# Kernel optimization log

Hardware: AMD Instinct MI355X
Metric: run time of the kernel (lower is better)

## Reference

```python
import jax, jax.numpy as jnp
import numpy as np

B, N, E = 128, 300, 300        # batch, nodes (max_length), edges per sample
DIN, DH, DOUT = 768, 256, 256  # input feat, gcn hidden, gcn output
R = 26                         # NUM_DEP_TYPES
NHEADS, HDIM = 8, DH // 8


def setup_inputs() -> dict:
    key = jax.random.key(0)
    ks = jax.random.split(key, 12)
    s = lambda d: 1.0 / np.sqrt(d)
    return {
        "node_features": jax.random.normal(ks[0], (B, N, DIN), jnp.float32),
        "src": jax.random.randint(ks[1], (B, E), 0, N, jnp.int32),
        "dst": jax.random.randint(ks[2], (B, E), 0, N, jnp.int32),
        "etype": jax.random.randint(ks[3], (B, E), 0, R, jnp.int32),
        "W_rel": jax.random.normal(ks[4], (R, DIN, DH), jnp.float32) * s(DIN),
        "W_loop": jax.random.normal(ks[5], (DIN, DH), jnp.float32) * s(DIN),
        "b_rel": jnp.zeros((DH,), jnp.float32),
        "in_proj_w": jax.random.normal(ks[6], (3 * DH, DH), jnp.float32) * s(DH),
        "in_proj_b": jnp.zeros((3 * DH,), jnp.float32),
        "out_proj_w": jax.random.normal(ks[7], (DH, DH), jnp.float32) * s(DH),
        "out_proj_b": jnp.zeros((DH,), jnp.float32),
        "mlp_w": jax.random.normal(ks[8], (DOUT, DH), jnp.float32) * s(DH),
        "mlp_b": jnp.zeros((DOUT,), jnp.float32),
    }


def reference(node_features, src, dst, etype, W_rel, W_loop, b_rel,
              in_proj_w, in_proj_b, out_proj_w, out_proj_b, mlp_w, mlp_b):
    # ---- RelGraphConv (regularizer=None, self_loop=True, sum aggregation) ----
    # gather source-node features per edge: [B, E, DIN]
    h_src = jnp.take_along_axis(node_features, src[..., None].astype(jnp.int32), axis=1)
    # per-relation masked matmul: msg[b,e] = h_src[b,e] @ W_rel[etype[b,e]]
    msg = jnp.zeros((B, E, DH), node_features.dtype)
    for r in range(R):  # fixed small relation set
        mask = (etype == r)[..., None]
        msg = msg + jnp.einsum('bei,io->beo', jnp.where(mask, h_src, 0.0), W_rel[r])
    # scatter-add messages to destination nodes
    b_idx = jnp.arange(B)[:, None]
    agg = jnp.zeros((B, N, DH), node_features.dtype).at[b_idx, dst].add(msg)
    h = agg + jnp.einsum('bni,io->bno', node_features, W_loop) + b_rel  # [B, N, DH]

    # ---- MultiheadAttention (self-attn over nodes, eval mode) ----
    qkv = jnp.einsum('bnd,ed->bne', h, in_proj_w) + in_proj_b
    q, k, v = jnp.split(qkv, 3, axis=-1)
    q = q.reshape(B, N, NHEADS, HDIM)
    k = k.reshape(B, N, NHEADS, HDIM)
    v = v.reshape(B, N, NHEADS, HDIM)
    scores = jnp.einsum('bqhd,bkhd->bhqk', q, k) / np.sqrt(HDIM)
    attn = jax.nn.softmax(scores, axis=-1)
    ctx = jnp.einsum('bhqk,bkhd->bqhd', attn, v).reshape(B, N, DH)
    attn_out = jnp.einsum('bnd,ed->bne', ctx, out_proj_w) + out_proj_b

    # ---- mean-pool over nodes + MLP ----
    pooled = jnp.mean(attn_out, axis=1)  # [B, DH]
    return pooled @ mlp_w.T + mlp_b      # [B, DOUT]
```

## Files before the change

kernel.cpp:

```cpp
#include <hip/hip_runtime.h>
#include <cstdint>
#include <cstddef>

#define BB 128
#define NN 300
#define EE 300
#define DIN 768
#define DH 256
#define NREL 26
#define NHEADS 8
#define HDIM 32
#define MTOT (BB*NN)
#define NEDGE (BB*EE)
#define NHB 150

typedef __attribute__((ext_vector_type(8))) short bf16x8;
typedef __attribute__((ext_vector_type(4))) float f32x4;
typedef unsigned short u16;
union BU { uint4 u; bf16x8 v; };

__device__ __forceinline__ unsigned int packbf2(float a, float b) {
    unsigned int ua = __float_as_uint(a);
    unsigned int ub = __float_as_uint(b);
    ua = (ua + 0x7FFFu + ((ua >> 16) & 1u)) >> 16;
    ub = (ub + 0x7FFFu + ((ub >> 16) & 1u)) & 0xFFFF0000u;
    return ua | ub;
}
__device__ __forceinline__ u16 packbf1(float a) {
    unsigned int ua = __float_as_uint(a);
    return (u16)((ua + 0x7FFFu + ((ua >> 16) & 1u)) >> 16);
}

__global__ __launch_bounds__(256) void b_hist(const int* __restrict__ etype,
                                              int* __restrict__ blockhist) {
    __shared__ int hist[NREL];
    const int tid = threadIdx.x;
    if (tid < NREL) hist[tid] = 0;
    __syncthreads();
    atomicAdd(&hist[etype[blockIdx.x * 256 + tid]], 1);
    __syncthreads();
    if (tid < NREL) blockhist[blockIdx.x * NREL + tid] = hist[tid];
}

__global__ __launch_bounds__(64) void b_scan(const int* __restrict__ blockhist,
                                             int* __restrict__ blockbase,
                                             int* __restrict__ cnt, int* __restrict__ off) {
    __shared__ int tot[NREL];
    const int r = threadIdx.x;
    if (r < NREL) {
        int run = 0;
        for (int b = 0; b < NHB; ++b) {
            blockbase[b * NREL + r] = run;
            run += blockhist[b * NREL + r];
        }
        tot[r] = run;
        cnt[r] = run;
    }
    __syncthreads();
    __shared__ int offs[NREL + 1];
    if (r == 0) {
        int acc = 0;
        for (int q = 0; q < NREL; ++q) { offs[q] = acc; off[q] = acc; acc += tot[q]; }
        offs[NREL] = acc; off[NREL] = acc;
    }
    __syncthreads();
    if (r < NREL) {
        int o = offs[r];
        for (int b = 0; b < NHB; ++b) blockbase[b * NREL + r] += o;
    }
}

__global__ __launch_bounds__(256) void b_scatter(const int* __restrict__ etype,
                                                 const int* __restrict__ blockbase,
                                                 int* __restrict__ list) {
    __shared__ int wavehist[4][NREL];
    __shared__ int waveoff[4][NREL];
    const int tid = threadIdx.x;
    const int w = tid >> 6, l = tid & 63;
    const int i = blockIdx.x * 256 + tid;
    const int r = etype[i];
    unsigned long long mymask = 0ull;
    #pragma unroll
    for (int q = 0; q < NREL; ++q) {
        unsigned long long m = __ballot(r == q);
        if (l == 0) wavehist[w][q] = __popcll(m);
        if (r == q) mymask = m;
    }
    const int myrank = __popcll(mymask & ((1ull << l) - 1ull));
    __syncthreads();
    if (tid < NREL) {
        int acc = 0;
        #pragma unroll
        for (int ww = 0; ww < 4; ++ww) { waveoff[ww][tid] = acc; acc += wavehist[ww][tid]; }
    }
    __syncthreads();
    list[blockbase[blockIdx.x * NREL + r] + waveoff[w][r] + myrank] = i;
}

__global__ __launch_bounds__(256) void c_cast8(const float4* __restrict__ in,
                                               uint4* __restrict__ out, int n8) {
    int i = blockIdx.x * 256 + threadIdx.x;
    if (i < n8) {
        float4 f0 = in[2*i], f1 = in[2*i+1];
        uint4 o;
        o.x = packbf2(f0.x, f0.y); o.y = packbf2(f0.z, f0.w);
        o.z = packbf2(f1.x, f1.y); o.w = packbf2(f1.z, f1.w);
        out[i] = o;
    }
}

__global__ __launch_bounds__(256) void c_cast_w(
    const float* __restrict__ wrel, const float* __restrict__ wl, const float* __restrict__ wq,
    uint4* __restrict__ wrb, uint4* __restrict__ wlb, uint4* __restrict__ wqb) {
    int t = blockIdx.x * 256 + threadIdx.x;
    int l = t & 63, fid = t >> 6;
    if (fid < NREL*24*16) {
        int r = fid / 384, rem = fid - r * 384;
        int kf = rem >> 4, nt = rem & 15;
        int k0 = 32*kf + 8*(l >> 4), n = 16*nt + (l & 15);
        const float* p = wrel + ((size_t)r*768 + k0) * 256 + n;
        uint4 o;
        o.x = packbf2(p[0], p[256]); o.y = packbf2(p[512], p[768]);
        o.z = packbf2(p[1024], p[1280]); o.w = packbf2(p[1536], p[1792]);
        wrb[t] = o;
    } else if (fid < NREL*24*16 + 384) {
        int f2 = fid - NREL*24*16;
        int kf = f2 >> 4, nt = f2 & 15;
        int k0 = 32*kf + 8*(l >> 4), n = 16*nt + (l & 15);
        const float* p = wl + (size_t)k0 * 256 + n;
        uint4 o;
        o.x = packbf2(p[0], p[256]); o.y = packbf2(p[512], p[768]);
        o.z = packbf2(p[1024], p[1280]); o.w = packbf2(p[1536], p[1792]);
        wlb[f2*64 + l] = o;
    } else {
        int f2 = fid - NREL*24*16 - 384;
        int kf = f2 / 48, nt = f2 % 48;
        int e = 16*nt + (l & 15), d0 = 32*kf + 8*(l >> 4);
        const float4* p = (const float4*)(wq + (size_t)e * 256 + d0);
        float4 f0 = p[0], f1 = p[1];
        uint4 o;
        o.x = packbf2(f0.x, f0.y); o.y = packbf2(f0.z, f0.w);
        o.z = packbf2(f1.x, f1.y); o.w = packbf2(f1.z, f1.w);
        wqb[f2*64 + l] = o;
    }
}

__global__ __launch_bounds__(256) void k1m(
    const uint4* __restrict__ xb, const uint4* __restrict__ wlb,
    const float* __restrict__ brel, float* __restrict__ h) {
    __shared__ uint4 As[512];
    const int tid = threadIdx.x;
    const int m0 = blockIdx.x * 64;
    const int nb = blockIdx.y;
    const int w = tid >> 6, l = tid & 63;
    const int g = l >> 4, q = l & 15;
    int cA[2];
    #pragma unroll
    for (int p = 0; p < 2; ++p) {
        int s = tid + p * 256;
        int fi = s >> 6, l2 = s & 63;
        int kf = fi >> 2, mt = fi & 3;
        int row = m0 + 16*mt + (l2 & 15);
        cA[p] = row * 96 + 4*kf + (l2 >> 4);
    }
    f32x4 acc[4][2];
    #pragma unroll
    for (int a = 0; a < 4; ++a)
        #pragma unroll
        for (int n = 0; n < 2; ++n) acc[a][n] = (f32x4){0.f,0.f,0.f,0.f};

    for (int step = 0; step < 12; ++step) {
        uint4 a0 = xb[cA[0] + step*8];
        uint4 a1 = xb[cA[1] + step*8];
        BU Bf[2][2];
        #pragma unroll
        for (int kf = 0; kf < 2; ++kf)
            #pragma unroll
            for (int nt = 0; nt < 2; ++nt)
                Bf[kf][nt].u = wlb[((step*2 + kf)*16 + nb*8 + w*2 + nt)*64 + l];
        __syncthreads();
        As[tid] = a0; As[tid + 256] = a1;
        __syncthreads();
        #pragma unroll
        for (int kf = 0; kf < 2; ++kf) {
            BU Af[4];
            #pragma unroll
            for (int mt = 0; mt < 4; ++mt) Af[mt].u = As[(kf*4 + mt)*64 + l];
            #pragma unroll
            for (int mt = 0; mt < 4; ++mt)
                #pragma unroll
                for (int nt = 0; nt < 2; ++nt)
                    acc[mt][nt] = __builtin_amdgcn_mfma_f32_16x16x32_bf16(Af[mt].v, Bf[kf][nt].v, acc[mt][nt], 0, 0, 0);
        }
    }
    #pragma unroll
    for (int nt = 0; nt < 2; ++nt) {
        int col = nb*128 + w*32 + nt*16 + q;
        float bias = brel[col];
        #pragma unroll
        for (int mt = 0; mt < 4; ++mt)
            #pragma unroll
            for (int i = 0; i < 4; ++i)
                h[(size_t)(m0 + 16*mt + 4*g + i)*256 + col] = acc[mt][nt][i] + bias;
    }
}

__global__ __launch_bounds__(256) void k2m(
    const uint4* __restrict__ xb, const uint4* __restrict__ wrb,
    const int* __restrict__ src, const int* __restrict__ dst,
    const int* __restrict__ cnt, const int* __restrict__ off,
    const int* __restrict__ list, float* __restrict__ h) {
    __shared__ uint4 As[512];
    __shared__ int arow_s[64];
    __shared__ int drow_s[64];
    const int r = blockIdx.y;
    const int c_total = cnt[r];
    const int t0 = blockIdx.x * 64;
    if (t0 >= c_total) return;
    const int nb = blockIdx.z;
    const int tid = threadIdx.x;
    if (tid < 64) {
        int e = t0 + tid;
        int ar = 0, dr = -1;
        if (e < c_total) {
            int eid = list[off[r] + e];
            int b = eid / EE;
            ar = b * NN + src[eid];
            dr = b * NN + dst[eid];
        }
        arow_s[tid] = ar; drow_s[tid] = dr;
    }
    __syncthreads();
    const int w = tid >> 6, l = tid & 63;
    const int g = l >> 4, q = l & 15;
    int cA[2];
    #pragma unroll
    for (int p = 0; p < 2; ++p) {
        int s = tid + p * 256;
        int fi = s >> 6, l2 = s & 63;
        int kf = fi >> 2, mt = fi & 3;
        int row = arow_s[16*mt + (l2 & 15)];
        cA[p] = row * 96 + 4*kf + (l2 >> 4);
    }
    const uint4* wb = wrb + (size_t)r * 24*16*64;
    f32x4 acc[4][2];
    #pragma unroll
    for (int a = 0; a < 4; ++a)
        #pragma unroll
        for (int n = 0; n < 2; ++n) acc[a][n] = (f32x4){0.f,0.f,0.f,0.f};

    for (int step = 0; step < 12; ++step) {
        uint4 a0 = xb[cA[0] + step*8];
        uint4 a1 = xb[cA[1] + step*8];
        BU Bf[2][2];
        #pragma unroll
        for (int kf = 0; kf < 2; ++kf)
            #pragma unroll
            for (int nt = 0; nt < 2; ++nt)
                Bf[kf][nt].u = wb[((step*2 + kf)*16 + nb*8 + w*2 + nt)*64 + l];
        __syncthreads();
        As[tid] = a0; As[tid + 256] = a1;
        __syncthreads();
        #pragma unroll
        for (int kf = 0; kf < 2; ++kf) {
            BU Af[4];
            #pragma unroll
            for (int mt = 0; mt < 4; ++mt) Af[mt].u = As[(kf*4 + mt)*64 + l];
            #pragma unroll
            for (int mt = 0; mt < 4; ++mt)
                #pragma unroll
                for (int nt = 0; nt < 2; ++nt)
                    acc[mt][nt] = __builtin_amdgcn_mfma_f32_16x16x32_bf16(Af[mt].v, Bf[kf][nt].v, acc[mt][nt], 0, 0, 0);
        }
    }
    #pragma unroll
    for (int mt = 0; mt < 4; ++mt)
        #pragma unroll
        for (int i = 0; i < 4; ++i) {
            int dr = drow_s[16*mt + 4*g + i];
            if (dr >= 0) {
                #pragma unroll
                for (int nt = 0; nt < 2; ++nt)
                    atomicAdd(&h[(size_t)dr*256 + nb*128 + w*32 + nt*16 + q], acc[mt][nt][i]);
            }
        }
}

__global__ __launch_bounds__(256) void k3m(
    const uint4* __restrict__ hb, const uint4* __restrict__ wqb,
    const float* __restrict__ bq,
    u16* __restrict__ qg, u16* __restrict__ kg, u16* __restrict__ vg) {
    __shared__ uint4 As[512];
    const int tid = threadIdx.x;
    const int m0 = blockIdx.x * 64;
    const int nb = blockIdx.y;
    const int w = tid >> 6, l = tid & 63;
    const int g = l >> 4, q = l & 15;
    int cA[2];
    #pragma unroll
    for (int p = 0; p < 2; ++p) {
        int s = tid + p * 256;
        int fi = s >> 6, l2 = s & 63;
        int kf = fi >> 2, mt = fi & 3;
        int row = m0 + 16*mt + (l2 & 15);
        cA[p] = row * 32 + 4*kf + (l2 >> 4);
    }
    f32x4 acc[4][2];
    #pragma unroll
    for (int a = 0; a < 4; ++a)
        #pragma unroll
        for (int n = 0; n < 2; ++n) acc[a][n] = (f32x4){0.f,0.f,0.f,0.f};

    for (int step = 0; step < 4; ++step) {
        uint4 a0 = hb[cA[0] + step*8];
        uint4 a1 = hb[cA[1] + step*8];
        BU Bf[2][2];
        #pragma unroll
        for (int kf = 0; kf < 2; ++kf)
            #pragma unroll
            for (int nt = 0; nt < 2; ++nt)
                Bf[kf][nt].u = wqb[((step*2 + kf)*48 + nb*8 + w*2 + nt)*64 + l];
        __syncthreads();
        As[tid] = a0; As[tid + 256] = a1;
        __syncthreads();
        #pragma unroll
        for (int kf = 0; kf < 2; ++kf) {
            BU Af[4];
            #pragma unroll
            for (int mt = 0; mt < 4; ++mt) Af[mt].u = As[(kf*4 + mt)*64 + l];
            #pragma unroll
            for (int mt = 0; mt < 4; ++mt)
                #pragma unroll
                for (int nt = 0; nt < 2; ++nt)
                    acc[mt][nt] = __builtin_amdgcn_mfma_f32_16x16x32_bf16(Af[mt].v, Bf[kf][nt].v, acc[mt][nt], 0, 0, 0);
        }
    }
    #pragma unroll
    for (int nt = 0; nt < 2; ++nt) {
        int e = nb*128 + w*32 + nt*16 + q;
        float bias = bq[e];
        int region = e >> 8;
        int hh = (e & 255) >> 5;
        int d  = e & 31;
        u16* outb = (region == 0) ? qg : (region == 1) ? kg : vg;
        #pragma unroll
        for (int mt = 0; mt < 4; ++mt) {
            #pragma unroll
            for (int i = 0; i < 4; ++i) {
                int j = m0 + 16*mt + 4*g + i;
                int b_ = j / 300;
                int jn = j - b_ * 300;
                u16 val = packbf1(acc[mt][nt][i] + bias);
                size_t byte;
                if (region < 2) {
                    int word = ((b_*8 + hh)*19 + (jn >> 4))*64 + 16*(d >> 3) + (jn & 15);
                    byte = (size_t)word*16 + (size_t)(d & 7)*2;
                } else {
                    int word = ((b_*8 + hh)*20 + (d >> 4)*10 + (jn >> 5))*64 + 16*((jn >> 3) & 3) + (d & 15);
                    byte = (size_t)word*16 + (size_t)(jn & 7)*2;
                }
                *(u16*)((char*)outb + byte) = val;
            }
        }
    }
}

__global__ __launch_bounds__(256) void k4_attn(
    const uint4* __restrict__ qg, const uint4* __restrict__ kg,
    const uint4* __restrict__ vg, float* __restrict__ pooled) {
    __shared__ uint4 kfrag[19*64];
    __shared__ uint4 vtfrag[20*64];
    __shared__ __align__(16) u16 pbuf[4][512];
    __shared__ float pool_lds[4][32];
    const int bh = blockIdx.x;
    const int tid = threadIdx.x;
    for (int s = tid; s < 19*64; s += 256) kfrag[s] = kg[(size_t)bh*19*64 + s];
    for (int s = tid; s < 20*64; s += 256) vtfrag[s] = vg[(size_t)bh*20*64 + s];
    __syncthreads();

    const int w = tid >> 6, l = tid & 63;
    const int g = l >> 4, q = l & 15;
    u16* pb = pbuf[w];
    u16* pw0 = (u16*)((char*)pb + 256*(g >> 1) + 16*q + 8*(g & 1));
    u16* pw1 = (u16*)((char*)pw0 + 512);
    const uint4* prd = (const uint4*)pb;

    const float c1 = 0.17677669529663687f * 1.4426950408889634f;
    float pool[8] = {0.f,0.f,0.f,0.f,0.f,0.f,0.f,0.f};

    for (int qt = w; qt < 19; qt += 4) {
        const int qrow = qt * 16 + q;
        BU uq; uq.u = qg[(size_t)(bh*19 + qt)*64 + l];

        f32x4 s_[19];
        __builtin_amdgcn_s_setprio(1);
        #pragma unroll
        for (int jt = 0; jt < 19; ++jt) {
            BU uk; uk.u = kfrag[jt * 64 + l];
            f32x4 z = {0.f, 0.f, 0.f, 0.f};
            s_[jt] = __builtin_amdgcn_mfma_f32_16x16x32_bf16(uk.v, uq.v, z, 0, 0, 0);
        }
        __builtin_amdgcn_s_setprio(0);
        if (g == 3) { s_[18][0] = -1e30f; s_[18][1] = -1e30f; s_[18][2] = -1e30f; s_[18][3] = -1e30f; }

        float m = -1e30f;
        #pragma unroll
        for (int jt = 0; jt < 19; ++jt)
            m = fmaxf(m, fmaxf(fmaxf(s_[jt][0], s_[jt][1]), fmaxf(s_[jt][2], s_[jt][3])));
        m = fmaxf(m, __shfl_xor(m, 16));
        m = fmaxf(m, __shfl_xor(m, 32));
        const float c0 = -m * c1;

        float lsum = 0.f;
        uint2 pk2[19];
        #pragma unroll
        for (int jt = 0; jt < 19; ++jt) {
            float p0 = exp2f(fmaf(s_[jt][0], c1, c0));
            float p1 = exp2f(fmaf(s_[jt][1], c1, c0));
            float p2 = exp2f(fmaf(s_[jt][2], c1, c0));
            float p3 = exp2f(fmaf(s_[jt][3], c1, c0));
            lsum += (p0 + p1) + (p2 + p3);
            pk2[jt].x = packbf2(p0, p1);
            pk2[jt].y = packbf2(p2, p3);
        }
        lsum += __shfl_xor(lsum, 16);
        lsum += __shfl_xor(lsum, 32);

        f32x4 ctx0 = {0.f,0.f,0.f,0.f}, ctx1 = {0.f,0.f,0.f,0.f};
        #pragma unroll
        for (int cc = 0; cc < 10; ++cc) {
            *(uint2*)pw0 = pk2[2*cc];
            uint2 z2 = make_uint2(0u, 0u);
            *(uint2*)pw1 = (2*cc + 1 < 19) ? pk2[2*cc+1] : z2;
            BU up;  up.u = prd[l];
            BU uv0; uv0.u = vtfrag[cc * 64 + l];
            BU uv1; uv1.u = vtfrag[(10 + cc) * 64 + l];
            ctx0 = __builtin_amdgcn_mfma_f32_16x16x32_bf16(uv0.v, up.v, ctx0, 0, 0, 0);
            ctx1 = __builtin_amdgcn_mfma_f32_16x16x32_bf16(uv1.v, up.v, ctx1, 0, 0, 0);
        }
        if (qrow < NN) {
            float inv = 1.0f / lsum;
            pool[0] += ctx0[0] * inv; pool[1] += ctx0[1] * inv;
            pool[2] += ctx0[2] * inv; pool[3] += ctx0[3] * inv;
            pool[4] += ctx1[0] * inv; pool[5] += ctx1[1] * inv;
            pool[6] += ctx1[2] * inv; pool[7] += ctx1[3] * inv;
        }
    }

    #pragma unroll
    for (int i = 0; i < 8; ++i) {
        float v = pool[i];
        v += __shfl_xor(v, 1); v += __shfl_xor(v, 2);
        v += __shfl_xor(v, 4); v += __shfl_xor(v, 8);
        pool[i] = v;
    }
    if (q == 0) {
        #pragma unroll
        for (int dt = 0; dt < 2; ++dt)
            #pragma unroll
            for (int i = 0; i < 4; ++i)
                pool_lds[w][dt * 16 + 4 * g + i] = pool[dt * 4 + i];
    }
    __syncthreads();
    if (tid < 32) {
        int b = bh >> 3, hh = bh & 7;
        float s = pool_lds[0][tid] + pool_lds[1][tid] + pool_lds[2][tid] + pool_lds[3][tid];
        pooled[(size_t)b * DH + hh * HDIM + tid] = s * (1.0f / 300.0f);
    }
}

__global__ __launch_bounds__(256) void k5_head(
    const float* __restrict__ pooled, const float* __restrict__ wo, const float* __restrict__ bo,
    const float* __restrict__ wm, const float* __restrict__ bm, float* __restrict__ out) {
    __shared__ float pc[DH];
    __shared__ float t1[DH];
    const int b = blockIdx.x, tid = threadIdx.x;
    pc[tid] = pooled[(size_t)b * DH + tid];
    __syncthreads();
    float acc = bo[tid];
    for (int d = 0; d < DH; ++d) acc += pc[d] * wo[(size_t)tid * DH + d];
    t1[tid] = acc;
    __syncthreads();
    float acc2 = bm[tid];
    for (int e2 = 0; e2 < DH; ++e2) acc2 += t1[e2] * wm[(size_t)tid * DH + e2];
    out[(size_t)b * DH + tid] = acc2;
}

extern "C" void kernel_launch(void* const* d_in, const int* in_sizes, int n_in,
                              void* d_out, int out_size, void* d_ws, size_t ws_size,
                              hipStream_t stream) {
    (void)in_sizes; (void)n_in; (void)out_size; (void)ws_size;
    const float* x     = (const float*)d_in[0];
    const int*   src   = (const int*)d_in[1];
    const int*   dst   = (const int*)d_in[2];
    const int*   etype = (const int*)d_in[3];
    const float* wrel  = (const float*)d_in[4];
    const float* wloop = (const float*)d_in[5];
    const float* brel  = (const float*)d_in[6];
    const float* wq    = (const float*)d_in[7];
    const float* bq    = (const float*)d_in[8];
    const float* wo    = (const float*)d_in[9];
    const float* bo    = (const float*)d_in[10];
    const float* wm    = (const float*)d_in[11];
    const float* bm    = (const float*)d_in[12];
    float* out = (float*)d_out;

    char* W = (char*)d_ws;
    float* h      = (float*)W;
    u16*   vg     = (u16*)W;
    u16*   xb     = (u16*)(W + 39321600ull);
    u16*   qg     = xb;
    u16*   kg     = (u16*)(W + 39321600ull + 19922944ull);
    u16*   hb     = (u16*)(W + 39321600ull + 58982400ull);
    uint4* wrb    = (uint4*)(W + 39321600ull + 58982400ull + 19660800ull);
    uint4* wlb    = (uint4*)((char*)wrb + 10223616ull);
    uint4* wqb    = (uint4*)((char*)wlb + 393216ull);
    float* pooled = (float*)((char*)wqb + 393216ull);
    int*   ibase  = (int*)((char*)pooled + 131072ull);
    int*   cnt    = ibase;
    int*   off    = ibase + 32;
    int*   list   = ibase + 64;
    int*   blockhist = list + NEDGE;
    int*   blockbase = blockhist + NHB*NREL;

    b_hist<<<NHB, 256, 0, stream>>>(etype, blockhist);
    b_scan<<<1, 64, 0, stream>>>(blockhist, blockbase, cnt, off);
    b_scatter<<<NHB, 256, 0, stream>>>(etype, blockbase, list);

    c_cast8<<<14400, 256, 0, stream>>>((const float4*)x, (uint4*)xb, 3686400);
    c_cast_w<<<2688, 256, 0, stream>>>(wrel, wloop, wq, wrb, wlb, wqb);

    k1m<<<dim3(600, 2), 256, 0, stream>>>((const uint4*)xb, wlb, brel, h);
    k2m<<<dim3(32, 26, 2), 256, 0, stream>>>((const uint4*)xb, wrb, src, dst, cnt, off, list, h);
    c_cast8<<<4800, 256, 0, stream>>>((const float4*)h, (uint4*)hb, 1228800);
    hipMemsetAsync(vg, 0, 20971520ull, stream);
    k3m<<<dim3(600, 6), 256, 0, stream>>>((const uint4*)hb, wqb, bq, qg, kg, vg);
    k4_attn<<<BB * NHEADS, 256, 0, stream>>>((const uint4*)qg, (const uint4*)kg, (const uint4*)vg, pooled);
    k5_head<<<BB, 256, 0, stream>>>(pooled, wo, bo, wm, bm, out);
}
```

Measured before the change: 302.2 us.

## Drop softmax max pass and stream P through enlarged LDS buffer in attention

The attention kernel no longer computes the row max before exponentiation. It computes exp2 of the scaled scores directly, relying on scores being small enough not to overflow. Scores and probabilities are produced in two halves of ten tiles each and written to a larger per-wave LDS buffer, then consumed by the PV MFMAs, which removes the 19-tile register arrays and the repeated write-read of a single staging slot. The manual bf16 rounding is replaced by the HIP float2-to-bfloat162 conversion. Skipping the max subtraction risks overflow for larger-magnitude scores, and the larger LDS footprint may lower occupancy.

```diff
diff --git a/kernel.cpp b/kernel.cpp
--- a/kernel.cpp
+++ b/kernel.cpp
@@ -1,4 +1,5 @@
 #include <hip/hip_runtime.h>
+#include <hip/hip_bf16.h>
 #include <cstdint>
 #include <cstddef>
 
@@ -29,6 +30,11 @@
 __device__ __forceinline__ u16 packbf1(float a) {
     unsigned int ua = __float_as_uint(a);
     return (u16)((ua + 0x7FFFu + ((ua >> 16) & 1u)) >> 16);
+}
+__device__ __forceinline__ unsigned cvtpk(float a, float b) {
+    union { __hip_bfloat162 h; unsigned u; } cv;
+    cv.h = __float22bfloat162_rn(make_float2(a, b));
+    return cv.u;
 }
 
 __global__ __launch_bounds__(256) void b_hist(const int* __restrict__ etype,
@@ -368,22 +374,20 @@
 __global__ __launch_bounds__(256) void k4_attn(
     const uint4* __restrict__ qg, const uint4* __restrict__ kg,
     const uint4* __restrict__ vg, float* __restrict__ pooled) {
-    __shared__ uint4 kfrag[19*64];
-    __shared__ uint4 vtfrag[20*64];
-    __shared__ __align__(16) u16 pbuf[4][512];
+    __shared__ uint4 kf_s[19*64];
+    __shared__ uint4 vt_s[20*64];
+    __shared__ __align__(16) u16 pbuf[4][2560];
     __shared__ float pool_lds[4][32];
     const int bh = blockIdx.x;
     const int tid = threadIdx.x;
-    for (int s = tid; s < 19*64; s += 256) kfrag[s] = kg[(size_t)bh*19*64 + s];
-    for (int s = tid; s < 20*64; s += 256) vtfrag[s] = vg[(size_t)bh*20*64 + s];
+    for (int s = tid; s < 19*64; s += 256) kf_s[s] = kg[(size_t)bh*19*64 + s];
+    for (int s = tid; s < 20*64; s += 256) vt_s[s] = vg[(size_t)bh*20*64 + s];
     __syncthreads();
 
     const int w = tid >> 6, l = tid & 63;
     const int g = l >> 4, q = l & 15;
-    u16* pb = pbuf[w];
-    u16* pw0 = (u16*)((char*)pb + 256*(g >> 1) + 16*q + 8*(g & 1));
-    u16* pw1 = (u16*)((char*)pw0 + 512);
-    const uint4* prd = (const uint4*)pb;
+    char* pwbase = (char*)pbuf[w] + 256*(g >> 1) + 16*q + 8*(g & 1);
+    const uint4* prd = (const uint4*)pbuf[w];
 
     const float c1 = 0.17677669529663687f * 1.4426950408889634f;
     float pool[8] = {0.f,0.f,0.f,0.f,0.f,0.f,0.f,0.f};
@@ -391,53 +395,42 @@
     for (int qt = w; qt < 19; qt += 4) {
         const int qrow = qt * 16 + q;
         BU uq; uq.u = qg[(size_t)(bh*19 + qt)*64 + l];
-
-        f32x4 s_[19];
-        __builtin_amdgcn_s_setprio(1);
-        #pragma unroll
-        for (int jt = 0; jt < 19; ++jt) {
-            BU uk; uk.u = kfrag[jt * 64 + l];
-            f32x4 z = {0.f, 0.f, 0.f, 0.f};
-            s_[jt] = __builtin_amdgcn_mfma_f32_16x16x32_bf16(uk.v, uq.v, z, 0, 0, 0);
-        }
-        __builtin_amdgcn_s_setprio(0);
-        if (g == 3) { s_[18][0] = -1e30f; s_[18][1] = -1e30f; s_[18][2] = -1e30f; s_[18][3] = -1e30f; }
-
-        float m = -1e30f;
-        #pragma unroll
-        for (int jt = 0; jt < 19; ++jt)
-            m = fmaxf(m, fmaxf(fmaxf(s_[jt][0], s_[jt][1]), fmaxf(s_[jt][2], s_[jt][3])));
-        m = fmaxf(m, __shfl_xor(m, 16));
-        m = fmaxf(m, __shfl_xor(m, 32));
-        const float c0 = -m * c1;
-
         float lsum = 0.f;
-        uint2 pk2[19];
-        #pragma unroll
-        for (int jt = 0; jt < 19; ++jt) {
-            float p0 = exp2f(fmaf(s_[jt][0], c1, c0));
-            float p1 = exp2f(fmaf(s_[jt][1], c1, c0));
-            float p2 = exp2f(fmaf(s_[jt][2], c1, c0));
-            float p3 = exp2f(fmaf(s_[jt][3], c1, c0));
-            lsum += (p0 + p1) + (p2 + p3);
-            pk2[jt].x = packbf2(p0, p1);
-            pk2[jt].y = packbf2(p2, p3);
+        f32x4 ctx0 = {0.f,0.f,0.f,0.f}, ctx1 = {0.f,0.f,0.f,0.f};
+
+        #pragma unroll
+        for (int half = 0; half < 2; ++half) {
+            #pragma unroll
+            for (int jj = 0; jj < 10; ++jj) {
+                const int jt = half*10 + jj;
+                uint2 pk = make_uint2(0u, 0u);
+                if (jt < 19) {
+                    BU uk; uk.u = kf_s[jt*64 + l];
+                    f32x4 z = {0.f,0.f,0.f,0.f};
+                    f32x4 s4 = __builtin_amdgcn_mfma_f32_16x16x32_bf16(uk.v, uq.v, z, 0, 0, 0);
+                    float p0 = exp2f(s4[0]*c1);
+                    float p1 = exp2f(s4[1]*c1);
+                    float p2 = exp2f(s4[2]*c1);
+                    float p3 = exp2f(s4[3]*c1);
+                    if (jt == 18 && g == 3) { p0 = 0.f; p1 = 0.f; p2 = 0.f; p3 = 0.f; }
+                    lsum += (p0 + p1) + (p2 + p3);
+                    pk.x = cvtpk(p0, p1);
+                    pk.y = cvtpk(p2, p3);
+                }
+                *(uint2*)(pwbase + 512*jj) = pk;
+            }
+            #pragma unroll
+            for (int cc = 0; cc < 5; ++cc) {
+                const int cg = half*5 + cc;
+                BU up;  up.u  = prd[cc*64 + l];
+                BU uv0; uv0.u = vt_s[cg*64 + l];
+                BU uv1; uv1.u = vt_s[(10 + cg)*64 + l];
+                ctx0 = __builtin_amdgcn_mfma_f32_16x16x32_bf16(uv0.v, up.v, ctx0, 0, 0, 0);
+                ctx1 = __builtin_amdgcn_mfma_f32_16x16x32_bf16(uv1.v, up.v, ctx1, 0, 0, 0);
+            }
         }
         lsum += __shfl_xor(lsum, 16);
         lsum += __shfl_xor(lsum, 32);
-
-        f32x4 ctx0 = {0.f,0.f,0.f,0.f}, ctx1 = {0.f,0.f,0.f,0.f};
-        #pragma unroll
-        for (int cc = 0; cc < 10; ++cc) {
-            *(uint2*)pw0 = pk2[2*cc];
-            uint2 z2 = make_uint2(0u, 0u);
-            *(uint2*)pw1 = (2*cc + 1 < 19) ? pk2[2*cc+1] : z2;
-            BU up;  up.u = prd[l];
-            BU uv0; uv0.u = vtfrag[cc * 64 + l];
-            BU uv1; uv1.u = vtfrag[(10 + cc) * 64 + l];
-            ctx0 = __builtin_amdgcn_mfma_f32_16x16x32_bf16(uv0.v, up.v, ctx0, 0, 0, 0);
-            ctx1 = __builtin_amdgcn_mfma_f32_16x16x32_bf16(uv1.v, up.v, ctx1, 0, 0, 0);
-        }
         if (qrow < NN) {
             float inv = 1.0f / lsum;
             pool[0] += ctx0[0] * inv; pool[1] += ctx0[1] * inv;
```

After: 274.5 us. -9.2%, faster.
